# Performance work log

Measured on AMD Instinct MI355X. Metric: run time of the kernel, lower is better.

The kernel has to match this reference:

```python
import jax, jax.numpy as jnp
import numpy as np

B, C, H, W = 4, 256, 64, 64
INTER = max(1, C // 8)  # 32


def setup_inputs() -> dict:
    key = jax.random.key(0)
    ks = jax.random.split(key, 8)
    s = 0.02  # conv weight init scale
    return {
        "feat": jax.random.normal(ks[0], (B, C, H, W), jnp.float32),
        "edge": jax.random.normal(ks[1], (B, C, H, W), jnp.float32),
        "wq": jax.random.normal(ks[2], (INTER, C), jnp.float32) * s,
        "bq": jnp.zeros((INTER,), jnp.float32),
        "wk": jax.random.normal(ks[3], (INTER, C), jnp.float32) * s,
        "bk": jnp.zeros((INTER,), jnp.float32),
        "wv": jax.random.normal(ks[4], (C, C), jnp.float32) * s,
        "bv": jnp.zeros((C,), jnp.float32),
    }


def reference(feat, edge, wq, bq, wk, bk, wv, bv):
    b, c, h, w = feat.shape
    n = h * w
    # 1x1 convs as channel matmuls; flatten spatial dims to n = H*W tokens
    q = (jnp.einsum('ic,bchw->bihw', wq, feat) + bq[None, :, None, None]).reshape(b, -1, n)  # [B, inter, N]
    k = (jnp.einsum('ic,bchw->bihw', wk, edge) + bk[None, :, None, None]).reshape(b, -1, n)  # [B, inter, N]
    v = (jnp.einsum('oc,bchw->bohw', wv, edge) + bv[None, :, None, None]).reshape(b, c, n)   # [B, C, N]
    # scores[b, nq, nk] = sum_i q[b,i,nq] * k[b,i,nk]; softmax over nk
    attn = jax.nn.softmax(jnp.einsum('bin,bim->bnm', q, k), axis=-1)  # [B, N, N]
    # out[b,c,nq] = sum_m v[b,c,m] * attn[b,nq,m]
    out = jnp.einsum('bcm,bnm->bcn', v, attn).reshape(b, c, h, w)
    return out + feat
```

## Files before the change

kernel.cpp:

```cpp
#include <hip/hip_runtime.h>
#include <cstddef>

#define BB 4
#define CC 256
#define NN 4096
#define NI 32

typedef __attribute__((ext_vector_type(8))) short bf16x8;
typedef __attribute__((ext_vector_type(16))) float f32x16;
typedef __attribute__((ext_vector_type(4))) float f32x4;
typedef unsigned short ushort_t;
typedef unsigned int uint32;

typedef union { uint32 u[4]; bf16x8 v; } fragU;

__device__ __forceinline__ uint32 f2bf_bits(float f) {
    union { float f; uint32 u; } v; v.f = f;
    return (v.u + 0x7fffu + ((v.u >> 16) & 1u)) >> 16;
}
__device__ __forceinline__ uint32 pack2bf(float a, float b) {
    return f2bf_bits(a) | (f2bf_bits(b) << 16);
}
__device__ __forceinline__ uint32 pack2bf_t(float a, float b) {
    union { float f; uint32 u; } A, B; A.f = a; B.f = b;
    return (B.u & 0xFFFF0000u) | (A.u >> 16);
}

__device__ __forceinline__ size_t vfidx(int b, int n, int c) {
    return ((((size_t)b * (NN / 16) + (n >> 4)) * 2 + ((n >> 3) & 1)) * (CC * 8))
           + (size_t)c * 8 + (n & 7);
}

__global__ __launch_bounds__(256) void wconv_kernel(
    const float* __restrict__ wq, const float* __restrict__ wk,
    const float* __restrict__ wv,
    ushort_t* __restrict__ wqF, ushort_t* __restrict__ wkF,
    ushort_t* __restrict__ wvF)
{
    const int bid = blockIdx.x;
    const int t = threadIdx.x;
    if (bid < 64) {
        const int fi = bid * 256 + t;
        const int o  = fi >> 6;
        const int k4 = (fi & 63) * 4;
        const f32x4 x = *(const f32x4*)&wv[(size_t)o * CC + k4];
        const int kkg = k4 >> 4, hh = (k4 >> 3) & 1, j0 = k4 & 7;
        const int ot = o >> 5, lane = hh * 32 + (o & 31);
        uint2 p; p.x = pack2bf(x[0], x[1]); p.y = pack2bf(x[2], x[3]);
        *(uint2*)&wvF[((size_t)(ot * 16 + kkg) * 64 + lane) * 8 + j0] = p;
    } else {
        const int which = (bid - 64) >> 1;
        const int part  = (bid - 64) & 1;
        const float* src = which ? wk : wq;
        ushort_t* dst = which ? wkF : wqF;
#pragma unroll
        for (int p = 0; p < 4; ++p) {
            const int fi = part * 1024 + p * 256 + t;
            const int o  = fi >> 6;
            const int k4 = (fi & 63) * 4;
            const f32x4 x = *(const f32x4*)&src[(size_t)o * CC + k4];
            const int kkg = k4 >> 4, hh = (k4 >> 3) & 1, j0 = k4 & 7;
            const int lane = hh * 32 + (o & 31);
            uint2 pr; pr.x = pack2bf(x[0], x[1]); pr.y = pack2bf(x[2], x[3]);
            *(uint2*)&dst[((size_t)kkg * 64 + lane) * 8 + j0] = pr;
        }
    }
}

__global__ __launch_bounds__(256, 1) void proj_kernel(
    const float* __restrict__ feat, const float* __restrict__ edge,
    const ushort_t* __restrict__ wqF, const ushort_t* __restrict__ wkF,
    const ushort_t* __restrict__ wvF,
    const float* __restrict__ bq, const float* __restrict__ bk,
    const float* __restrict__ bv,
    ushort_t* __restrict__ qT, ushort_t* __restrict__ kT,
    ushort_t* __restrict__ vF)
{
    __shared__ __attribute__((aligned(16))) uint32 sF[4][2][64][4];
    __shared__ __attribute__((aligned(16))) uint32 sE[4][2][64][4];

    const int tid = threadIdx.x;
    const int b = blockIdx.y;
    const int n0 = blockIdx.x * 64;
    const int w = tid >> 6, lane = tid & 63;
    const int col = lane & 31, h = lane >> 5;

    const ushort_t* __restrict__ aQK = ((w < 2) ? wqF : wkF) + (size_t)lane * 8;
    const ushort_t* __restrict__ wvB0 = wvF + ((size_t)((2 * w + 0) * 16) * 64 + lane) * 8;
    const ushort_t* __restrict__ wvB1 = wvF + ((size_t)((2 * w + 1) * 16) * 64 + lane) * 8;
    const uint32* __restrict__ bSrc =
        (w == 0) ? &sF[0][0][lane][0] :
        (w == 1) ? &sF[0][1][lane][0] :
        (w == 2) ? &sE[0][0][lane][0] : &sE[0][1][lane][0];

    f32x16 accV[2][2];
    f32x16 accS;
#pragma unroll
    for (int r = 0; r < 16; ++r) {
        accS[r] = 0.f;
        accV[0][0][r] = 0.f; accV[0][1][r] = 0.f;
        accV[1][0][r] = 0.f; accV[1][1][r] = 0.f;
    }

    f32x4 rF[2][2], rE[2][2];

#pragma unroll
    for (int p = 0; p < 2; ++p) {
        const int pi = p * 256 + tid;
        const int m = pi >> 4, cidx = pi & 15;
        const size_t ga = ((size_t)(b * CC + 2 * m)) * NN + n0 + cidx * 4;
        rF[p][0] = *(const f32x4*)&feat[ga];
        rF[p][1] = *(const f32x4*)&feat[ga + NN];
        rE[p][0] = *(const f32x4*)&edge[ga];
        rE[p][1] = *(const f32x4*)&edge[ga + NN];
    }

    for (int ch = 0; ch < 4; ++ch) {
#pragma unroll
        for (int p = 0; p < 2; ++p) {
            const int pi = p * 256 + tid;
            const int m = pi >> 4, cidx = pi & 15;
            const int kk = m >> 3, hh = (m >> 2) & 1, ju = m & 3;
#pragma unroll
            for (int c = 0; c < 4; ++c) {
                const int cn = cidx * 4 + c;
                const int nt = cn >> 5, cl = cn & 31;
                sF[kk][nt][hh * 32 + cl][ju] = pack2bf(rF[p][0][c], rF[p][1][c]);
                sE[kk][nt][hh * 32 + cl][ju] = pack2bf(rE[p][0][c], rE[p][1][c]);
            }
        }
        __syncthreads();

        if (ch < 3) {
            const int c0 = (ch + 1) * 64;
#pragma unroll
            for (int p = 0; p < 2; ++p) {
                const int pi = p * 256 + tid;
                const int m = pi >> 4, cidx = pi & 15;
                const size_t ga = ((size_t)(b * CC + c0 + 2 * m)) * NN + n0 + cidx * 4;
                rF[p][0] = *(const f32x4*)&feat[ga];
                rF[p][1] = *(const f32x4*)&feat[ga + NN];
                rE[p][0] = *(const f32x4*)&edge[ga];
                rE[p][1] = *(const f32x4*)&edge[ga + NN];
            }
        }

#pragma unroll
        for (int kk = 0; kk < 4; ++kk) {
            const int kkg = ch * 4 + kk;
            const bf16x8 eA0 = *(const bf16x8*)&sE[kk][0][lane][0];
            const bf16x8 eA1 = *(const bf16x8*)&sE[kk][1][lane][0];
            const bf16x8 vB0 = *(const bf16x8*)&wvB0[(size_t)kkg * 512];
            const bf16x8 vB1 = *(const bf16x8*)&wvB1[(size_t)kkg * 512];
            const bf16x8 aS  = *(const bf16x8*)&aQK[(size_t)kkg * 512];
            const bf16x8 bS  = *(const bf16x8*)&bSrc[(size_t)kk * 512];
            accS = __builtin_amdgcn_mfma_f32_32x32x16_bf16(aS, bS, accS, 0, 0, 0);
            accV[0][0] = __builtin_amdgcn_mfma_f32_32x32x16_bf16(eA0, vB0, accV[0][0], 0, 0, 0);
            accV[0][1] = __builtin_amdgcn_mfma_f32_32x32x16_bf16(eA0, vB1, accV[0][1], 0, 0, 0);
            accV[1][0] = __builtin_amdgcn_mfma_f32_32x32x16_bf16(eA1, vB0, accV[1][0], 0, 0, 0);
            accV[1][1] = __builtin_amdgcn_mfma_f32_32x32x16_bf16(eA1, vB1, accV[1][1], 0, 0, 0);
        }
        __syncthreads();
    }

    {
        const float* bias = (w < 2) ? bq : bk;
        ushort_t* dst = (w < 2) ? qT : kT;
        const int nt = w & 1;
        const size_t base = ((size_t)b * NN + n0 + nt * 32 + col) * NI;
#pragma unroll
        for (int q = 0; q < 4; ++q) {
            const int i0 = 8 * q + 4 * h;
            const float x0 = accS[4 * q + 0] + bias[i0 + 0];
            const float x1 = accS[4 * q + 1] + bias[i0 + 1];
            const float x2 = accS[4 * q + 2] + bias[i0 + 2];
            const float x3 = accS[4 * q + 3] + bias[i0 + 3];
            uint2 pr; pr.x = pack2bf(x0, x1); pr.y = pack2bf(x2, x3);
            *(uint2*)&dst[base + i0] = pr;
        }
    }

#pragma unroll
    for (int cti = 0; cti < 2; ++cti) {
        const int o = (2 * w + cti) * 32 + col;
        const float vb = bv[o];
#pragma unroll
        for (int mt = 0; mt < 2; ++mt) {
#pragma unroll
            for (int q = 0; q < 4; ++q) {
                const int nst = n0 + mt * 32 + 8 * q + 4 * h;
                uint2 pr;
                pr.x = pack2bf(accV[mt][cti][4 * q + 0] + vb,
                               accV[mt][cti][4 * q + 1] + vb);
                pr.y = pack2bf(accV[mt][cti][4 * q + 2] + vb,
                               accV[mt][cti][4 * q + 3] + vb);
                *(uint2*)&vF[vfidx(b, nst, o)] = pr;
            }
        }
    }
}

__global__ __launch_bounds__(512, 2) void attn_kernel(
    const ushort_t* __restrict__ qT, const ushort_t* __restrict__ kT,
    const ushort_t* __restrict__ vF, const float* __restrict__ feat,
    float* __restrict__ out)
{
    __shared__ float red[4][64][33];
    __shared__ float lpart[4][2][32];
    __shared__ float linvS[64];

    const int tid  = threadIdx.x;
    const int b    = blockIdx.y;
    const int nq0  = blockIdx.x * 64;
    const int w    = tid >> 6;
    const int lane = tid & 63;
    const int col  = lane & 31;
    const int h    = lane >> 5;
    const int qs   = w & 1;
    const int kg   = w >> 1;

    bf16x8 bQ0, bQ1;
    {
        const size_t qb = ((size_t)b * NN + nq0 + qs * 32 + col) * NI + h * 8;
        bQ0 = *(const bf16x8*)&qT[qb];
        bQ1 = *(const bf16x8*)&qT[qb + 16];
    }

    f32x16 acc[8];
#pragma unroll
    for (int cs = 0; cs < 8; ++cs)
#pragma unroll
        for (int r = 0; r < 16; ++r) acc[cs][r] = 0.f;

    float lp = 0.f;

    const size_t kTb = (size_t)b * NN * NI;
    const int keybase = kg * 1024;

    for (int strip = 0; strip < 32; ++strip) {
        const int key0 = keybase + strip * 32;

        const size_t kb = kTb + (size_t)(key0 + col) * NI + h * 8;
        const bf16x8 aK0 = *(const bf16x8*)&kT[kb];
        const bf16x8 aK1 = *(const bf16x8*)&kT[kb + 16];

        f32x16 st;
#pragma unroll
        for (int r = 0; r < 16; ++r) st[r] = 0.f;
        st = __builtin_amdgcn_mfma_f32_32x32x16_bf16(aK0, bQ0, st, 0, 0, 0);
        st = __builtin_amdgcn_mfma_f32_32x32x16_bf16(aK1, bQ1, st, 0, 0, 0);

        float p[16]; float sum = 0.f;
#pragma unroll
        for (int r = 0; r < 16; ++r) { p[r] = __expf(st[r]); sum += p[r]; }
        lp += sum;

        uint32 pk[8];
#pragma unroll
        for (int j = 0; j < 8; ++j) pk[j] = pack2bf_t(p[2 * j], p[2 * j + 1]);
        uint32 rv[8];
#pragma unroll
        for (int j = 0; j < 8; ++j) rv[j] = __shfl_xor(pk[j], 32, 64);
        fragU F0, F1;
        F0.u[0] = h ? rv[2] : pk[0];
        F0.u[1] = h ? rv[3] : pk[1];
        F0.u[2] = h ? pk[2] : rv[0];
        F0.u[3] = h ? pk[3] : rv[1];
        F1.u[0] = h ? rv[6] : pk[4];
        F1.u[1] = h ? rv[7] : pk[5];
        F1.u[2] = h ? pk[6] : rv[4];
        F1.u[3] = h ? pk[7] : rv[5];

        const size_t vbB = (((size_t)b * (NN / 16) + (key0 >> 4)) * 2 + h) * (CC * 8)
                         + (size_t)col * 8;
#pragma unroll
        for (int cs = 0; cs < 8; ++cs) {
            const bf16x8 v0 = *(const bf16x8*)&vF[vbB + cs * 256];
            const bf16x8 v1 = *(const bf16x8*)&vF[vbB + 4096 + cs * 256];
            acc[cs] = __builtin_amdgcn_mfma_f32_32x32x16_bf16(F0.v, v0, acc[cs], 0, 0, 0);
            acc[cs] = __builtin_amdgcn_mfma_f32_32x32x16_bf16(F1.v, v1, acc[cs], 0, 0, 0);
        }
    }

    lp += __shfl_xor(lp, 32, 64);
    if (h == 0) lpart[kg][qs][col] = lp;
    __syncthreads();
    if (tid < 64) {
        const int s = tid >> 5, q = tid & 31;
        linvS[tid] = 1.0f / (lpart[0][s][q] + lpart[1][s][q] + lpart[2][s][q] + lpart[3][s][q]);
    }
    __syncthreads();

    const int c32 = tid >> 4;
    const int q4  = (tid & 15) * 4;
    float lv[4];
#pragma unroll
    for (int j = 0; j < 4; ++j) lv[j] = linvS[q4 + j];

#pragma unroll
    for (int pp = 0; pp < 8; ++pp) {
#pragma unroll
        for (int r = 0; r < 16; ++r) {
            const int row = qs * 32 + (r & 3) + 8 * (r >> 2) + 4 * h;
            red[kg][row][col] = acc[pp][r];
        }
        __syncthreads();
        {
            const int cglob = pp * 32 + c32;
            const size_t gb = ((size_t)b * CC + cglob) * NN + nq0 + q4;
            float o[4];
#pragma unroll
            for (int j = 0; j < 4; ++j)
                o[j] = red[0][q4 + j][c32] + red[1][q4 + j][c32]
                     + red[2][q4 + j][c32] + red[3][q4 + j][c32];
            const float4 f4 = *(const float4*)&feat[gb];
            float4 o4;
            o4.x = o[0] * lv[0] + f4.x;
            o4.y = o[1] * lv[1] + f4.y;
            o4.z = o[2] * lv[2] + f4.z;
            o4.w = o[3] * lv[3] + f4.w;
            *(float4*)&out[gb] = o4;
        }
        __syncthreads();
    }
}

extern "C" void kernel_launch(void* const* d_in, const int* in_sizes, int n_in,
                              void* d_out, int out_size, void* d_ws, size_t ws_size,
                              hipStream_t stream)
{
    (void)in_sizes; (void)n_in; (void)out_size; (void)ws_size;
    const float* feat = (const float*)d_in[0];
    const float* edge = (const float*)d_in[1];
    const float* wq   = (const float*)d_in[2];
    const float* bq   = (const float*)d_in[3];
    const float* wk   = (const float*)d_in[4];
    const float* bk   = (const float*)d_in[5];
    const float* wv   = (const float*)d_in[6];
    const float* bv   = (const float*)d_in[7];
    float* out = (float*)d_out;

    ushort_t* qT  = (ushort_t*)d_ws;
    ushort_t* kT  = qT + (size_t)BB * NN * NI;
    ushort_t* vF  = kT + (size_t)BB * NN * NI;

    ushort_t* wvF = (ushort_t*)d_out;
    ushort_t* wqF = wvF + (size_t)CC * CC;
    ushort_t* wkF = wqF + (size_t)NI * CC;

    wconv_kernel<<<dim3(68), 256, 0, stream>>>(wq, wk, wv, wqF, wkF, wvF);
    proj_kernel<<<dim3(NN / 64, BB), 256, 0, stream>>>(feat, edge, wqF, wkF, wvF,
                                                       bq, bk, bv, qT, kT, vF);
    attn_kernel<<<dim3(NN / 64, BB), 512, 0, stream>>>(qT, kT, vF, feat, out);
}
```

Before: 152.4 us.

## Fuse weight conversion, projection and attention into one kernel with grid barriers

Merges the three separate launches into one persistent kernel of 256 blocks that moves between phases through atomic-counter grid barriers. The aim is to remove inter-kernel launch gaps and tail drain between weight conversion, projection and attention. The projection phase is reworked for 512 threads, with eight waves each computing half of the V tiles and only four waves doing the Q/K projection. The cost is that correctness now depends on all blocks being co-resident at once, and each barrier adds spin-wait latency.

```diff
diff --git a/kernel.cpp b/kernel.cpp
--- a/kernel.cpp
+++ b/kernel.cpp
@@ -5,6 +5,7 @@
 #define CC 256
 #define NN 4096
 #define NI 32
+#define NBLK 256
 
 typedef __attribute__((ext_vector_type(8))) short bf16x8;
 typedef __attribute__((ext_vector_type(16))) float f32x16;
@@ -14,6 +15,8 @@
 
 typedef union { uint32 u[4]; bf16x8 v; } fragU;
 
+__device__ uint32 g_bar[2];
+
 __device__ __forceinline__ uint32 f2bf_bits(float f) {
     union { float f; uint32 u; } v; v.f = f;
     return (v.u + 0x7fffu + ((v.u >> 16) & 1u)) >> 16;
@@ -31,297 +34,285 @@
            + (size_t)c * 8 + (n & 7);
 }
 
-__global__ __launch_bounds__(256) void wconv_kernel(
-    const float* __restrict__ wq, const float* __restrict__ wk,
-    const float* __restrict__ wv,
+__device__ __forceinline__ void grid_barrier(uint32* bar) {
+    __threadfence();
+    __syncthreads();
+    if (threadIdx.x == 0) {
+        const uint32 t = __hip_atomic_fetch_add(bar, 1u, __ATOMIC_ACQ_REL,
+                                                __HIP_MEMORY_SCOPE_AGENT);
+        const uint32 goal = (t / NBLK + 1u) * NBLK;
+        while ((int)(__hip_atomic_load(bar, __ATOMIC_ACQUIRE,
+                                       __HIP_MEMORY_SCOPE_AGENT) - goal) < 0)
+            __builtin_amdgcn_s_sleep(2);
+    }
+    __syncthreads();
+    __threadfence();
+}
+
+__global__ __launch_bounds__(512, 2) void fused_kernel(
+    const float* __restrict__ feat, const float* __restrict__ edge,
+    const float* __restrict__ wq, const float* __restrict__ bq,
+    const float* __restrict__ wk, const float* __restrict__ bk,
+    const float* __restrict__ wv, const float* __restrict__ bv,
+    ushort_t* __restrict__ qT, ushort_t* __restrict__ kT,
+    ushort_t* __restrict__ vF,
     ushort_t* __restrict__ wqF, ushort_t* __restrict__ wkF,
-    ushort_t* __restrict__ wvF)
+    ushort_t* __restrict__ wvF,
+    float* __restrict__ out)
 {
-    const int bid = blockIdx.x;
-    const int t = threadIdx.x;
-    if (bid < 64) {
-        const int fi = bid * 256 + t;
-        const int o  = fi >> 6;
-        const int k4 = (fi & 63) * 4;
-        const f32x4 x = *(const f32x4*)&wv[(size_t)o * CC + k4];
-        const int kkg = k4 >> 4, hh = (k4 >> 3) & 1, j0 = k4 & 7;
-        const int ot = o >> 5, lane = hh * 32 + (o & 31);
-        uint2 p; p.x = pack2bf(x[0], x[1]); p.y = pack2bf(x[2], x[3]);
-        *(uint2*)&wvF[((size_t)(ot * 16 + kkg) * 64 + lane) * 8 + j0] = p;
-    } else {
-        const int which = (bid - 64) >> 1;
-        const int part  = (bid - 64) & 1;
-        const float* src = which ? wk : wq;
-        ushort_t* dst = which ? wkF : wqF;
-#pragma unroll
-        for (int p = 0; p < 4; ++p) {
-            const int fi = part * 1024 + p * 256 + t;
+    __shared__ __attribute__((aligned(16))) uint32 sF[4][2][64][4];
+    __shared__ __attribute__((aligned(16))) uint32 sE[4][2][64][4];
+    __shared__ float red[4][64][33];
+    __shared__ float lpart[4][2][32];
+    __shared__ float linvS[64];
+
+    const int tid = threadIdx.x;
+    const int b   = blockIdx.y;
+    const int n0  = blockIdx.x * 64;
+
+    {
+        const int gf = (b * 64 + blockIdx.x) * 512 + tid;
+        if (gf < 16384) {
+            const int fi = gf;
+            const int o  = fi >> 6;
+            const int k4 = (fi & 63) * 4;
+            const f32x4 x = *(const f32x4*)&wv[(size_t)o * CC + k4];
+            const int kkg = k4 >> 4, hh = (k4 >> 3) & 1, j0 = k4 & 7;
+            const int ot = o >> 5, ln = hh * 32 + (o & 31);
+            uint2 p; p.x = pack2bf(x[0], x[1]); p.y = pack2bf(x[2], x[3]);
+            *(uint2*)&wvF[((size_t)(ot * 16 + kkg) * 64 + ln) * 8 + j0] = p;
+        } else if (gf < 20480) {
+            const int fi = (gf - 16384) & 2047;
+            const float* src = (gf < 18432) ? wq : wk;
+            ushort_t* dst = (gf < 18432) ? wqF : wkF;
             const int o  = fi >> 6;
             const int k4 = (fi & 63) * 4;
             const f32x4 x = *(const f32x4*)&src[(size_t)o * CC + k4];
             const int kkg = k4 >> 4, hh = (k4 >> 3) & 1, j0 = k4 & 7;
-            const int lane = hh * 32 + (o & 31);
-            uint2 pr; pr.x = pack2bf(x[0], x[1]); pr.y = pack2bf(x[2], x[3]);
-            *(uint2*)&dst[((size_t)kkg * 64 + lane) * 8 + j0] = pr;
+            const int ln = hh * 32 + (o & 31);
+            uint2 p; p.x = pack2bf(x[0], x[1]); p.y = pack2bf(x[2], x[3]);
+            *(uint2*)&dst[((size_t)kkg * 64 + ln) * 8 + j0] = p;
         }
     }
-}
-
-__global__ __launch_bounds__(256, 1) void proj_kernel(
-    const float* __restrict__ feat, const float* __restrict__ edge,
-    const ushort_t* __restrict__ wqF, const ushort_t* __restrict__ wkF,
-    const ushort_t* __restrict__ wvF,
-    const float* __restrict__ bq, const float* __restrict__ bk,
-    const float* __restrict__ bv,
-    ushort_t* __restrict__ qT, ushort_t* __restrict__ kT,
-    ushort_t* __restrict__ vF)
-{
-    __shared__ __attribute__((aligned(16))) uint32 sF[4][2][64][4];
-    __shared__ __attribute__((aligned(16))) uint32 sE[4][2][64][4];
-
-    const int tid = threadIdx.x;
-    const int b = blockIdx.y;
-    const int n0 = blockIdx.x * 64;
-    const int w = tid >> 6, lane = tid & 63;
-    const int col = lane & 31, h = lane >> 5;
-
-    const ushort_t* __restrict__ aQK = ((w < 2) ? wqF : wkF) + (size_t)lane * 8;
-    const ushort_t* __restrict__ wvB0 = wvF + ((size_t)((2 * w + 0) * 16) * 64 + lane) * 8;
-    const ushort_t* __restrict__ wvB1 = wvF + ((size_t)((2 * w + 1) * 16) * 64 + lane) * 8;
-    const uint32* __restrict__ bSrc =
-        (w == 0) ? &sF[0][0][lane][0] :
-        (w == 1) ? &sF[0][1][lane][0] :
-        (w == 2) ? &sE[0][0][lane][0] : &sE[0][1][lane][0];
-
-    f32x16 accV[2][2];
-    f32x16 accS;
-#pragma unroll
-    for (int r = 0; r < 16; ++r) {
-        accS[r] = 0.f;
-        accV[0][0][r] = 0.f; accV[0][1][r] = 0.f;
-        accV[1][0][r] = 0.f; accV[1][1][r] = 0.f;
-    }
-
-    f32x4 rF[2][2], rE[2][2];
-
-#pragma unroll
-    for (int p = 0; p < 2; ++p) {
-        const int pi = p * 256 + tid;
-        const int m = pi >> 4, cidx = pi & 15;
-        const size_t ga = ((size_t)(b * CC + 2 * m)) * NN + n0 + cidx * 4;
-        rF[p][0] = *(const f32x4*)&feat[ga];
-        rF[p][1] = *(const f32x4*)&feat[ga + NN];
-        rE[p][0] = *(const f32x4*)&edge[ga];
-        rE[p][1] = *(const f32x4*)&edge[ga + NN];
-    }
-
-    for (int ch = 0; ch < 4; ++ch) {
-#pragma unroll
-        for (int p = 0; p < 2; ++p) {
-            const int pi = p * 256 + tid;
-            const int m = pi >> 4, cidx = pi & 15;
-            const int kk = m >> 3, hh = (m >> 2) & 1, ju = m & 3;
+    grid_barrier(&g_bar[0]);
+
+    {
+        const int w8   = tid >> 6, lane = tid & 63;
+        const int col  = lane & 31, h = lane >> 5;
+        const int mt   = w8 >> 2;
+        const int ct0  = (w8 & 3) * 2;
+
+        const ushort_t* __restrict__ aQK  = ((w8 < 2) ? wqF : wkF) + (size_t)lane * 8;
+        const ushort_t* __restrict__ wvB0 = wvF + ((size_t)((ct0 + 0) * 16) * 64 + lane) * 8;
+        const ushort_t* __restrict__ wvB1 = wvF + ((size_t)((ct0 + 1) * 16) * 64 + lane) * 8;
+        const uint32* __restrict__ bSrc =
+            (w8 == 0) ? &sF[0][0][lane][0] :
+            (w8 == 1) ? &sF[0][1][lane][0] :
+            (w8 == 2) ? &sE[0][0][lane][0] : &sE[0][1][lane][0];
+
+        f32x16 accV0, accV1, accS;
+#pragma unroll
+        for (int r = 0; r < 16; ++r) { accV0[r] = 0.f; accV1[r] = 0.f; accS[r] = 0.f; }
+
+        const int m = tid >> 4, cidx = tid & 15;
+        const int kkw = m >> 3, hh = (m >> 2) & 1, ju = m & 3;
+        f32x4 rF0, rF1, rE0, rE1;
+        {
+            const size_t ga = ((size_t)(b * CC + 2 * m)) * NN + n0 + cidx * 4;
+            rF0 = *(const f32x4*)&feat[ga]; rF1 = *(const f32x4*)&feat[ga + NN];
+            rE0 = *(const f32x4*)&edge[ga]; rE1 = *(const f32x4*)&edge[ga + NN];
+        }
+
+        for (int ch = 0; ch < 4; ++ch) {
 #pragma unroll
             for (int c = 0; c < 4; ++c) {
                 const int cn = cidx * 4 + c;
                 const int nt = cn >> 5, cl = cn & 31;
-                sF[kk][nt][hh * 32 + cl][ju] = pack2bf(rF[p][0][c], rF[p][1][c]);
-                sE[kk][nt][hh * 32 + cl][ju] = pack2bf(rE[p][0][c], rE[p][1][c]);
-            }
-        }
-        __syncthreads();
-
-        if (ch < 3) {
-            const int c0 = (ch + 1) * 64;
-#pragma unroll
-            for (int p = 0; p < 2; ++p) {
-                const int pi = p * 256 + tid;
-                const int m = pi >> 4, cidx = pi & 15;
-                const size_t ga = ((size_t)(b * CC + c0 + 2 * m)) * NN + n0 + cidx * 4;
-                rF[p][0] = *(const f32x4*)&feat[ga];
-                rF[p][1] = *(const f32x4*)&feat[ga + NN];
-                rE[p][0] = *(const f32x4*)&edge[ga];
-                rE[p][1] = *(const f32x4*)&edge[ga + NN];
-            }
-        }
-
-#pragma unroll
-        for (int kk = 0; kk < 4; ++kk) {
-            const int kkg = ch * 4 + kk;
-            const bf16x8 eA0 = *(const bf16x8*)&sE[kk][0][lane][0];
-            const bf16x8 eA1 = *(const bf16x8*)&sE[kk][1][lane][0];
-            const bf16x8 vB0 = *(const bf16x8*)&wvB0[(size_t)kkg * 512];
-            const bf16x8 vB1 = *(const bf16x8*)&wvB1[(size_t)kkg * 512];
-            const bf16x8 aS  = *(const bf16x8*)&aQK[(size_t)kkg * 512];
-            const bf16x8 bS  = *(const bf16x8*)&bSrc[(size_t)kk * 512];
-            accS = __builtin_amdgcn_mfma_f32_32x32x16_bf16(aS, bS, accS, 0, 0, 0);
-            accV[0][0] = __builtin_amdgcn_mfma_f32_32x32x16_bf16(eA0, vB0, accV[0][0], 0, 0, 0);
-            accV[0][1] = __builtin_amdgcn_mfma_f32_32x32x16_bf16(eA0, vB1, accV[0][1], 0, 0, 0);
-            accV[1][0] = __builtin_amdgcn_mfma_f32_32x32x16_bf16(eA1, vB0, accV[1][0], 0, 0, 0);
-            accV[1][1] = __builtin_amdgcn_mfma_f32_32x32x16_bf16(eA1, vB1, accV[1][1], 0, 0, 0);
-        }
-        __syncthreads();
-    }
-
-    {
-        const float* bias = (w < 2) ? bq : bk;
-        ushort_t* dst = (w < 2) ? qT : kT;
-        const int nt = w & 1;
-        const size_t base = ((size_t)b * NN + n0 + nt * 32 + col) * NI;
-#pragma unroll
-        for (int q = 0; q < 4; ++q) {
-            const int i0 = 8 * q + 4 * h;
-            const float x0 = accS[4 * q + 0] + bias[i0 + 0];
-            const float x1 = accS[4 * q + 1] + bias[i0 + 1];
-            const float x2 = accS[4 * q + 2] + bias[i0 + 2];
-            const float x3 = accS[4 * q + 3] + bias[i0 + 3];
-            uint2 pr; pr.x = pack2bf(x0, x1); pr.y = pack2bf(x2, x3);
-            *(uint2*)&dst[base + i0] = pr;
-        }
-    }
-
-#pragma unroll
-    for (int cti = 0; cti < 2; ++cti) {
-        const int o = (2 * w + cti) * 32 + col;
-        const float vb = bv[o];
-#pragma unroll
-        for (int mt = 0; mt < 2; ++mt) {
+                sF[kkw][nt][hh * 32 + cl][ju] = pack2bf(rF0[c], rF1[c]);
+                sE[kkw][nt][hh * 32 + cl][ju] = pack2bf(rE0[c], rE1[c]);
+            }
+            __syncthreads();
+
+            if (ch < 3) {
+                const size_t ga = ((size_t)(b * CC + (ch + 1) * 64 + 2 * m)) * NN
+                                + n0 + cidx * 4;
+                rF0 = *(const f32x4*)&feat[ga]; rF1 = *(const f32x4*)&feat[ga + NN];
+                rE0 = *(const f32x4*)&edge[ga]; rE1 = *(const f32x4*)&edge[ga + NN];
+            }
+
+#pragma unroll
+            for (int kk = 0; kk < 4; ++kk) {
+                const int kkg = ch * 4 + kk;
+                const bf16x8 eA  = *(const bf16x8*)&sE[kk][mt][lane][0];
+                const bf16x8 vB0 = *(const bf16x8*)&wvB0[(size_t)kkg * 512];
+                const bf16x8 vB1 = *(const bf16x8*)&wvB1[(size_t)kkg * 512];
+                accV0 = __builtin_amdgcn_mfma_f32_32x32x16_bf16(eA, vB0, accV0, 0, 0, 0);
+                accV1 = __builtin_amdgcn_mfma_f32_32x32x16_bf16(eA, vB1, accV1, 0, 0, 0);
+                if (w8 < 4) {
+                    const bf16x8 aS = *(const bf16x8*)&aQK[(size_t)kkg * 512];
+                    const bf16x8 bS = *(const bf16x8*)&bSrc[(size_t)kk * 512];
+                    accS = __builtin_amdgcn_mfma_f32_32x32x16_bf16(aS, bS, accS, 0, 0, 0);
+                }
+            }
+            __syncthreads();
+        }
+
+        if (w8 < 4) {
+            const float* bias = (w8 < 2) ? bq : bk;
+            ushort_t* dst = (w8 < 2) ? qT : kT;
+            const int nt = w8 & 1;
+            const size_t base = ((size_t)b * NN + n0 + nt * 32 + col) * NI;
+#pragma unroll
+            for (int q = 0; q < 4; ++q) {
+                const int i0 = 8 * q + 4 * h;
+                const float x0 = accS[4 * q + 0] + bias[i0 + 0];
+                const float x1 = accS[4 * q + 1] + bias[i0 + 1];
+                const float x2 = accS[4 * q + 2] + bias[i0 + 2];
+                const float x3 = accS[4 * q + 3] + bias[i0 + 3];
+                uint2 pr; pr.x = pack2bf(x0, x1); pr.y = pack2bf(x2, x3);
+                *(uint2*)&dst[base + i0] = pr;
+            }
+        }
+
+        {
+            const int o0 = (ct0 + 0) * 32 + col;
+            const float vb0 = bv[o0];
 #pragma unroll
             for (int q = 0; q < 4; ++q) {
                 const int nst = n0 + mt * 32 + 8 * q + 4 * h;
                 uint2 pr;
-                pr.x = pack2bf(accV[mt][cti][4 * q + 0] + vb,
-                               accV[mt][cti][4 * q + 1] + vb);
-                pr.y = pack2bf(accV[mt][cti][4 * q + 2] + vb,
-                               accV[mt][cti][4 * q + 3] + vb);
-                *(uint2*)&vF[vfidx(b, nst, o)] = pr;
+                pr.x = pack2bf(accV0[4 * q + 0] + vb0, accV0[4 * q + 1] + vb0);
+                pr.y = pack2bf(accV0[4 * q + 2] + vb0, accV0[4 * q + 3] + vb0);
+                *(uint2*)&vF[vfidx(b, nst, o0)] = pr;
+            }
+            const int o1 = (ct0 + 1) * 32 + col;
+            const float vb1 = bv[o1];
+#pragma unroll
+            for (int q = 0; q < 4; ++q) {
+                const int nst = n0 + mt * 32 + 8 * q + 4 * h;
+                uint2 pr;
+                pr.x = pack2bf(accV1[4 * q + 0] + vb1, accV1[4 * q + 1] + vb1);
+                pr.y = pack2bf(accV1[4 * q + 2] + vb1, accV1[4 * q + 3] + vb1);
+                *(uint2*)&vF[vfidx(b, nst, o1)] = pr;
             }
         }
     }
-}
-
-__global__ __launch_bounds__(512, 2) void attn_kernel(
-    const ushort_t* __restrict__ qT, const ushort_t* __restrict__ kT,
-    const ushort_t* __restrict__ vF, const float* __restrict__ feat,
-    float* __restrict__ out)
-{
-    __shared__ float red[4][64][33];
-    __shared__ float lpart[4][2][32];
-    __shared__ float linvS[64];
-
-    const int tid  = threadIdx.x;
-    const int b    = blockIdx.y;
-    const int nq0  = blockIdx.x * 64;
-    const int w    = tid >> 6;
-    const int lane = tid & 63;
-    const int col  = lane & 31;
-    const int h    = lane >> 5;
-    const int qs   = w & 1;
-    const int kg   = w >> 1;
-
-    bf16x8 bQ0, bQ1;
+    grid_barrier(&g_bar[1]);
+
     {
-        const size_t qb = ((size_t)b * NN + nq0 + qs * 32 + col) * NI + h * 8;
-        bQ0 = *(const bf16x8*)&qT[qb];
-        bQ1 = *(const bf16x8*)&qT[qb + 16];
-    }
-
-    f32x16 acc[8];
-#pragma unroll
-    for (int cs = 0; cs < 8; ++cs)
-#pragma unroll
-        for (int r = 0; r < 16; ++r) acc[cs][r] = 0.f;
-
-    float lp = 0.f;
-
-    const size_t kTb = (size_t)b * NN * NI;
-    const int keybase = kg * 1024;
-
-    for (int strip = 0; strip < 32; ++strip) {
-        const int key0 = keybase + strip * 32;
-
-        const size_t kb = kTb + (size_t)(key0 + col) * NI + h * 8;
-        const bf16x8 aK0 = *(const bf16x8*)&kT[kb];
-        const bf16x8 aK1 = *(const bf16x8*)&kT[kb + 16];
-
-        f32x16 st;
-#pragma unroll
-        for (int r = 0; r < 16; ++r) st[r] = 0.f;
-        st = __builtin_amdgcn_mfma_f32_32x32x16_bf16(aK0, bQ0, st, 0, 0, 0);
-        st = __builtin_amdgcn_mfma_f32_32x32x16_bf16(aK1, bQ1, st, 0, 0, 0);
-
-        float p[16]; float sum = 0.f;
-#pragma unroll
-        for (int r = 0; r < 16; ++r) { p[r] = __expf(st[r]); sum += p[r]; }
-        lp += sum;
-
-        uint32 pk[8];
-#pragma unroll
-        for (int j = 0; j < 8; ++j) pk[j] = pack2bf_t(p[2 * j], p[2 * j + 1]);
-        uint32 rv[8];
-#pragma unroll
-        for (int j = 0; j < 8; ++j) rv[j] = __shfl_xor(pk[j], 32, 64);
-        fragU F0, F1;
-        F0.u[0] = h ? rv[2] : pk[0];
-        F0.u[1] = h ? rv[3] : pk[1];
-        F0.u[2] = h ? pk[2] : rv[0];
-        F0.u[3] = h ? pk[3] : rv[1];
-        F1.u[0] = h ? rv[6] : pk[4];
-        F1.u[1] = h ? rv[7] : pk[5];
-        F1.u[2] = h ? pk[6] : rv[4];
-        F1.u[3] = h ? pk[7] : rv[5];
-
-        const size_t vbB = (((size_t)b * (NN / 16) + (key0 >> 4)) * 2 + h) * (CC * 8)
-                         + (size_t)col * 8;
-#pragma unroll
-        for (int cs = 0; cs < 8; ++cs) {
-            const bf16x8 v0 = *(const bf16x8*)&vF[vbB + cs * 256];
-            const bf16x8 v1 = *(const bf16x8*)&vF[vbB + 4096 + cs * 256];
-            acc[cs] = __builtin_amdgcn_mfma_f32_32x32x16_bf16(F0.v, v0, acc[cs], 0, 0, 0);
-            acc[cs] = __builtin_amdgcn_mfma_f32_32x32x16_bf16(F1.v, v1, acc[cs], 0, 0, 0);
-        }
-    }
-
-    lp += __shfl_xor(lp, 32, 64);
-    if (h == 0) lpart[kg][qs][col] = lp;
-    __syncthreads();
-    if (tid < 64) {
-        const int s = tid >> 5, q = tid & 31;
-        linvS[tid] = 1.0f / (lpart[0][s][q] + lpart[1][s][q] + lpart[2][s][q] + lpart[3][s][q]);
-    }
-    __syncthreads();
-
-    const int c32 = tid >> 4;
-    const int q4  = (tid & 15) * 4;
-    float lv[4];
-#pragma unroll
-    for (int j = 0; j < 4; ++j) lv[j] = linvS[q4 + j];
-
-#pragma unroll
-    for (int pp = 0; pp < 8; ++pp) {
-#pragma unroll
-        for (int r = 0; r < 16; ++r) {
-            const int row = qs * 32 + (r & 3) + 8 * (r >> 2) + 4 * h;
-            red[kg][row][col] = acc[pp][r];
-        }
+        const int nq0  = n0;
+        const int w    = tid >> 6;
+        const int lane = tid & 63;
+        const int col  = lane & 31;
+        const int h    = lane >> 5;
+        const int qs   = w & 1;
+        const int kg   = w >> 1;
+
+        bf16x8 bQ0, bQ1;
+        {
+            const size_t qb = ((size_t)b * NN + nq0 + qs * 32 + col) * NI + h * 8;
+            bQ0 = *(const bf16x8*)&qT[qb];
+            bQ1 = *(const bf16x8*)&qT[qb + 16];
+        }
+
+        f32x16 acc[8];
+#pragma unroll
+        for (int cs = 0; cs < 8; ++cs)
+#pragma unroll
+            for (int r = 0; r < 16; ++r) acc[cs][r] = 0.f;
+
+        float lp = 0.f;
+
+        const size_t kTb = (size_t)b * NN * NI;
+        const int keybase = kg * 1024;
+
+        for (int strip = 0; strip < 32; ++strip) {
+            const int key0 = keybase + strip * 32;
+
+            const size_t kb = kTb + (size_t)(key0 + col) * NI + h * 8;
+            const bf16x8 aK0 = *(const bf16x8*)&kT[kb];
+            const bf16x8 aK1 = *(const bf16x8*)&kT[kb + 16];
+
+            f32x16 st;
+#pragma unroll
+            for (int r = 0; r < 16; ++r) st[r] = 0.f;
+            st = __builtin_amdgcn_mfma_f32_32x32x16_bf16(aK0, bQ0, st, 0, 0, 0);
+            st = __builtin_amdgcn_mfma_f32_32x32x16_bf16(aK1, bQ1, st, 0, 0, 0);
+
+            float p[16]; float sum = 0.f;
+#pragma unroll
+            for (int r = 0; r < 16; ++r) { p[r] = __expf(st[r]); sum += p[r]; }
+            lp += sum;
+
+            uint32 pk[8];
+#pragma unroll
+            for (int j = 0; j < 8; ++j) pk[j] = pack2bf_t(p[2 * j], p[2 * j + 1]);
+            uint32 rv[8];
+#pragma unroll
+            for (int j = 0; j < 8; ++j) rv[j] = __shfl_xor(pk[j], 32, 64);
+            fragU F0, F1;
+            F0.u[0] = h ? rv[2] : pk[0];
+            F0.u[1] = h ? rv[3] : pk[1];
+            F0.u[2] = h ? pk[2] : rv[0];
+            F0.u[3] = h ? pk[3] : rv[1];
+            F1.u[0] = h ? rv[6] : pk[4];
+            F1.u[1] = h ? rv[7] : pk[5];
+            F1.u[2] = h ? pk[6] : rv[4];
+            F1.u[3] = h ? pk[7] : rv[5];
+
+            const size_t vbB = (((size_t)b * (NN / 16) + (key0 >> 4)) * 2 + h) * (CC * 8)
+                             + (size_t)col * 8;
+#pragma unroll
+            for (int cs = 0; cs < 8; ++cs) {
+                const bf16x8 v0 = *(const bf16x8*)&vF[vbB + cs * 256];
+                const bf16x8 v1 = *(const bf16x8*)&vF[vbB + 4096 + cs * 256];
+                acc[cs] = __builtin_amdgcn_mfma_f32_32x32x16_bf16(F0.v, v0, acc[cs], 0, 0, 0);
+                acc[cs] = __builtin_amdgcn_mfma_f32_32x32x16_bf16(F1.v, v1, acc[cs], 0, 0, 0);
+            }
+        }
+
+        lp += __shfl_xor(lp, 32, 64);
+        if (h == 0) lpart[kg][qs][col] = lp;
         __syncthreads();
-        {
-            const int cglob = pp * 32 + c32;
-            const size_t gb = ((size_t)b * CC + cglob) * NN + nq0 + q4;
-            float o[4];
-#pragma unroll
-            for (int j = 0; j < 4; ++j)
-                o[j] = red[0][q4 + j][c32] + red[1][q4 + j][c32]
-                     + red[2][q4 + j][c32] + red[3][q4 + j][c32];
-            const float4 f4 = *(const float4*)&feat[gb];
-            float4 o4;
-            o4.x = o[0] * lv[0] + f4.x;
-            o4.y = o[1] * lv[1] + f4.y;
-            o4.z = o[2] * lv[2] + f4.z;
-            o4.w = o[3] * lv[3] + f4.w;
-            *(float4*)&out[gb] = o4;
+        if (tid < 64) {
+            const int s = tid >> 5, q = tid & 31;
+            linvS[tid] = 1.0f / (lpart[0][s][q] + lpart[1][s][q]
+                               + lpart[2][s][q] + lpart[3][s][q]);
         }
         __syncthreads();
+
+        const int c32 = tid >> 4;
+        const int q4  = (tid & 15) * 4;
+        float lv[4];
+#pragma unroll
+        for (int j = 0; j < 4; ++j) lv[j] = linvS[q4 + j];
+
+#pragma unroll
+        for (int pp = 0; pp < 8; ++pp) {
+#pragma unroll
+            for (int r = 0; r < 16; ++r) {
+                const int row = qs * 32 + (r & 3) + 8 * (r >> 2) + 4 * h;
+                red[kg][row][col] = acc[pp][r];
+            }
+            __syncthreads();
+            {
+                const int cglob = pp * 32 + c32;
+                const size_t gb = ((size_t)b * CC + cglob) * NN + nq0 + q4;
+                float o[4];
+#pragma unroll
+                for (int j = 0; j < 4; ++j)
+                    o[j] = red[0][q4 + j][c32] + red[1][q4 + j][c32]
+                         + red[2][q4 + j][c32] + red[3][q4 + j][c32];
+                const float4 f4 = *(const float4*)&feat[gb];
+                float4 o4;
+                o4.x = o[0] * lv[0] + f4.x;
+                o4.y = o[1] * lv[1] + f4.y;
+                o4.z = o[2] * lv[2] + f4.z;
+                o4.w = o[3] * lv[3] + f4.w;
+                *(float4*)&out[gb] = o4;
+            }
+            __syncthreads();
+        }
     }
 }
 
@@ -348,8 +339,7 @@
     ushort_t* wqF = wvF + (size_t)CC * CC;
     ushort_t* wkF = wqF + (size_t)NI * CC;
 
-    wconv_kernel<<<dim3(68), 256, 0, stream>>>(wq, wk, wv, wqF, wkF, wvF);
-    proj_kernel<<<dim3(NN / 64, BB), 256, 0, stream>>>(feat, edge, wqF, wkF, wvF,
-                                                       bq, bk, bv, qT, kT, vF);
-    attn_kernel<<<dim3(NN / 64, BB), 512, 0, stream>>>(qT, kT, vF, feat, out);
-}
+    fused_kernel<<<dim3(NN / 64, BB), 512, 0, stream>>>(
+        feat, edge, wq, bq, wk, bk, wv, bv,
+        qT, kT, vF, wqF, wkF, wvF, out);
+}
```

Result: slower. 341.0 us (+123.8%).
